# Optimization experiments

Hardware: AMD Instinct MI355X
Metric: run time of the kernel (lower is better)

## Reference

```python
import jax, jax.numpy as jnp
import numpy as np

B, T, D, H, O = 64, 4096, 256, 256, 256

def setup_inputs() -> dict:
    key = jax.random.key(0)
    kx, k1, k2, k3 = jax.random.split(key, 4)
    return {
        "x": jax.random.normal(kx, (B, T, D), dtype=jnp.float32),
        "h0": jnp.zeros((B, H), dtype=jnp.float32),
        "W_xh": jax.random.normal(k1, (D, H), dtype=jnp.float32) * 0.1,
        "W_hh": jax.random.normal(k2, (H, H), dtype=jnp.float32) * 0.1,
        "b_h": jnp.zeros((H,), dtype=jnp.float32),
        "W_hy": jax.random.normal(k3, (H, O), dtype=jnp.float32) * 0.1,
        "b_y": jnp.zeros((O,), dtype=jnp.float32),
    }

def reference(x, h0, W_xh, W_hh, b_h, W_hy, b_y):
    # Precompute input projection for all timesteps: (T, B, H)
    xp = jnp.einsum("btd,dh->tbh", x, W_xh) + b_h

    def step(h, xp_t):
        h_t = jnp.tanh(xp_t + h @ W_hh)  # (B, H)
        return h_t, h_t

    h_final, hs = jax.lax.scan(step, h0, xp)  # hs: (T, B, H)
    outputs = jnp.einsum("tbh,ho->bto", hs, W_hy) + b_y  # (B, T, O)
    return outputs, h_final
```

## Files before the change

### kernel.cpp

```cpp
#include <hip/hip_runtime.h>
#include <hip/hip_bf16.h>
#include <stdint.h>

#define TT 4096
#define BBATCH 64
#define DD 256
#define HH 256
#define OO 256

typedef float  f32x4  __attribute__((ext_vector_type(4)));
typedef short  bf16x8 __attribute__((ext_vector_type(8)));

__device__ __forceinline__ unsigned short f2bf(float f) {
  unsigned u = __float_as_uint(f);
  u += 0x7FFFu + ((u >> 16) & 1u);
  return (unsigned short)(u >> 16);
}
__device__ __forceinline__ float bf2f(unsigned short h) {
  return __uint_as_float(((unsigned)h) << 16);
}

__global__ void k0_transpose(const float* __restrict__ Wxh, const float* __restrict__ Why,
                             unsigned short* __restrict__ Wt1, unsigned short* __restrict__ Wt2) {
  const int n = blockIdx.x & 255;
  const int k = threadIdx.x;
  if (blockIdx.x < 256) Wt1[n * 256 + k] = f2bf(Wxh[k * 256 + n]);
  else                  Wt2[n * 256 + k] = f2bf(Why[k * 256 + n]);
}

__global__ __launch_bounds__(256) void k1_gemm_xp(
    const float* __restrict__ x, const unsigned short* __restrict__ Wt,
    const float* __restrict__ bh, unsigned short* __restrict__ xp) {
  __shared__ __align__(16) unsigned short As[64 * 264];
  const int tid = threadIdx.x;
  const int m0 = blockIdx.x * 64;

  #pragma unroll
  for (int rr = 0; rr < 16; ++rr) {
    int idx = tid + rr * 256;
    int row = idx >> 6;
    int c4  = (idx & 63) << 2;
    f32x4 v = *(const f32x4*)(x + (size_t)(m0 + row) * 256 + c4);
    unsigned w0 = (unsigned)f2bf(v[0]) | ((unsigned)f2bf(v[1]) << 16);
    unsigned w1 = (unsigned)f2bf(v[2]) | ((unsigned)f2bf(v[3]) << 16);
    *(uint2*)(As + row * 264 + c4) = make_uint2(w0, w1);
  }

  const int wv = tid >> 6, ln = tid & 63, l15 = ln & 15, q = ln >> 4;

  bf16x8 bfr[4][8];
  #pragma unroll
  for (int ntl = 0; ntl < 4; ++ntl) {
    #pragma unroll
    for (int kt = 0; kt < 8; ++kt) {
      int n = (wv * 4 + ntl) * 16 + l15;
      int k = kt * 32 + q * 8;
      bfr[ntl][kt] = *(const bf16x8*)(Wt + n * 256 + k);
    }
  }
  float biasv[4];
  #pragma unroll
  for (int ntl = 0; ntl < 4; ++ntl) biasv[ntl] = bh[(wv * 4 + ntl) * 16 + l15];

  __syncthreads();

  #pragma unroll 1
  for (int ms = 0; ms < 4; ++ms) {
    bf16x8 afr[8];
    #pragma unroll
    for (int kt = 0; kt < 8; ++kt)
      afr[kt] = *(const bf16x8*)(As + (ms * 16 + l15) * 264 + kt * 32 + q * 8);
    f32x4 acc[4];
    #pragma unroll
    for (int ntl = 0; ntl < 4; ++ntl) acc[ntl] = (f32x4){0.f, 0.f, 0.f, 0.f};
    #pragma unroll
    for (int ntl = 0; ntl < 4; ++ntl) {
      #pragma unroll
      for (int kt = 0; kt < 8; ++kt)
        acc[ntl] = __builtin_amdgcn_mfma_f32_16x16x32_bf16(afr[kt], bfr[ntl][kt], acc[ntl], 0, 0, 0);
    }
    #pragma unroll
    for (int ntl = 0; ntl < 4; ++ntl) {
      int c = (wv * 4 + ntl) * 16 + l15;
      #pragma unroll
      for (int r = 0; r < 4; ++r) {
        int m = m0 + ms * 16 + q * 4 + r;
        int t = m & 4095, b = m >> 12;
        xp[(size_t)(t * 64 + b) * 256 + c] = f2bf(acc[ntl][r] + biasv[ntl]);
      }
    }
  }
}

__global__ __launch_bounds__(512) void k2_rnn(
    unsigned short* xp_hs,
    const float* __restrict__ h0, const float* __restrict__ Whh,
    float* __restrict__ hfin) {
  __shared__ float hbuf[256];
  __shared__ float part[8][256];
  const int tid = threadIdx.x;
  const int b   = blockIdx.x;
  const int ig  = tid >> 6;
  const int jg  = tid & 63;

  float w[32][4];
  #pragma unroll
  for (int i = 0; i < 32; ++i)
    *(f32x4*)w[i] = *(const f32x4*)(Whh + (size_t)(32 * ig + i) * 256 + 4 * jg);

  float xpv = 0.f;
  if (tid < 256) {
    hbuf[tid] = h0[b * 256 + tid];
    xpv = bf2f(xp_hs[(size_t)b * 256 + tid]);
  }
  __syncthreads();

  #pragma unroll 1
  for (int t = 0; t < 4096; ++t) {
    float hv = hbuf[32 * ig + (tid & 31)];
    float a0 = 0.f, a1 = 0.f, a2 = 0.f, a3 = 0.f;
    #pragma unroll
    for (int i = 0; i < 32; ++i) {
      float s = __uint_as_float((unsigned)__builtin_amdgcn_readlane(__float_as_uint(hv), i));
      a0 = fmaf(s, w[i][0], a0);
      a1 = fmaf(s, w[i][1], a1);
      a2 = fmaf(s, w[i][2], a2);
      a3 = fmaf(s, w[i][3], a3);
    }
    *(f32x4*)&part[ig][4 * jg] = (f32x4){a0, a1, a2, a3};
    __syncthreads();
    if (tid < 256) {
      float s = part[0][tid] + part[1][tid] + part[2][tid] + part[3][tid]
              + part[4][tid] + part[5][tid] + part[6][tid] + part[7][tid] + xpv;
      float e  = __expf(2.f * s);
      float hn = 1.f - 2.f / (e + 1.f);
      hbuf[tid] = hn;
      xp_hs[(size_t)(t * 64 + b) * 256 + tid] = f2bf(hn);
      if (t < 4095)
        xpv = bf2f(xp_hs[(size_t)((t + 1) * 64 + b) * 256 + tid]);
    }
    __syncthreads();
  }
  if (tid < 256) hfin[b * 256 + tid] = hbuf[tid];
}

__global__ __launch_bounds__(256) void k3_gemm_out(
    const unsigned short* __restrict__ hs, const unsigned short* __restrict__ Wt,
    const float* __restrict__ by, float* __restrict__ out) {
  __shared__ __align__(16) unsigned short As[64 * 264];
  const int tid = threadIdx.x;
  const int m0 = blockIdx.x * 64;

  #pragma unroll
  for (int rr = 0; rr < 8; ++rr) {
    int idx = tid + rr * 256;
    int row = idx >> 5;
    int c8  = (idx & 31) << 3;
    *(uint4*)(As + row * 264 + c8) = *(const uint4*)(hs + (size_t)(m0 + row) * 256 + c8);
  }

  const int wv = tid >> 6, ln = tid & 63, l15 = ln & 15, q = ln >> 4;

  bf16x8 bfr[4][8];
  #pragma unroll
  for (int ntl = 0; ntl < 4; ++ntl) {
    #pragma unroll
    for (int kt = 0; kt < 8; ++kt) {
      int n = (wv * 4 + ntl) * 16 + l15;
      int k = kt * 32 + q * 8;
      bfr[ntl][kt] = *(const bf16x8*)(Wt + n * 256 + k);
    }
  }
  float biasv[4];
  #pragma unroll
  for (int ntl = 0; ntl < 4; ++ntl) biasv[ntl] = by[(wv * 4 + ntl) * 16 + l15];

  __syncthreads();

  #pragma unroll 1
  for (int ms = 0; ms < 4; ++ms) {
    bf16x8 afr[8];
    #pragma unroll
    for (int kt = 0; kt < 8; ++kt)
      afr[kt] = *(const bf16x8*)(As + (ms * 16 + l15) * 264 + kt * 32 + q * 8);
    f32x4 acc[4];
    #pragma unroll
    for (int ntl = 0; ntl < 4; ++ntl) acc[ntl] = (f32x4){0.f, 0.f, 0.f, 0.f};
    #pragma unroll
    for (int ntl = 0; ntl < 4; ++ntl) {
      #pragma unroll
      for (int kt = 0; kt < 8; ++kt)
        acc[ntl] = __builtin_amdgcn_mfma_f32_16x16x32_bf16(afr[kt], bfr[ntl][kt], acc[ntl], 0, 0, 0);
    }
    #pragma unroll
    for (int ntl = 0; ntl < 4; ++ntl) {
      int c = (wv * 4 + ntl) * 16 + l15;
      #pragma unroll
      for (int r = 0; r < 4; ++r) {
        int m  = m0 + ms * 16 + q * 4 + r;
        int bb = m & 63, t = m >> 6;
        out[(size_t)(bb * 4096 + t) * 256 + c] = acc[ntl][r] + biasv[ntl];
      }
    }
  }
}

extern "C" void kernel_launch(void* const* d_in, const int* in_sizes, int n_in,
                              void* d_out, int out_size, void* d_ws, size_t ws_size,
                              hipStream_t stream) {
  const float* x   = (const float*)d_in[0];
  const float* h0  = (const float*)d_in[1];
  const float* Wxh = (const float*)d_in[2];
  const float* Whh = (const float*)d_in[3];
  const float* bh  = (const float*)d_in[4];
  const float* Why = (const float*)d_in[5];
  const float* by  = (const float*)d_in[6];
  float* out = (float*)d_out;

  unsigned short* xp  = (unsigned short*)d_ws;
  unsigned short* Wt1 = xp + (size_t)TT * BBATCH * HH;
  unsigned short* Wt2 = Wt1 + 256 * 256;
  float* hfin = out + (size_t)BBATCH * TT * OO;

  hipLaunchKernelGGL(k0_transpose, dim3(512), dim3(256), 0, stream, Wxh, Why, Wt1, Wt2);
  hipLaunchKernelGGL(k1_gemm_xp,  dim3(4096), dim3(256), 0, stream, x, Wt1, bh, xp);
  hipLaunchKernelGGL(k2_rnn,      dim3(64),   dim3(512), 0, stream, xp, h0, Whh, hfin);
  hipLaunchKernelGGL(k3_gemm_out, dim3(4096), dim3(256), 0, stream, xp, Wt2, by, out);
}
```

Before: 4.793 ms.

## Run RNN recurrence on MFMA with 16 batches per block

Replaces the per-batch scalar-FMA recurrence kernel (64 blocks of 512 threads, one batch each, two barriers per step) with an MFMA-based kernel. Each of 4 blocks handles 16 batch rows, keeps the transposed bf16 W_hh in registers, and double-buffers the hidden state in LDS so each step needs only one barrier. The kernel also prefetches the next step's input projection and uses a reciprocal-based tanh. The trade is far fewer CUs in use and bf16 hidden-state precision in the recurrence, in exchange for much less per-step instruction and synchronisation cost.

After: 4.864 ms. Within noise of the previous version (+1.5%).

```diff
diff --git a/kernel.cpp b/kernel.cpp
--- a/kernel.cpp
+++ b/kernel.cpp
@@ -10,6 +10,7 @@
 
 typedef float  f32x4  __attribute__((ext_vector_type(4)));
 typedef short  bf16x8 __attribute__((ext_vector_type(8)));
+typedef unsigned short u16x4 __attribute__((ext_vector_type(4)));
 
 __device__ __forceinline__ unsigned short f2bf(float f) {
   unsigned u = __float_as_uint(f);
@@ -19,13 +20,25 @@
 __device__ __forceinline__ float bf2f(unsigned short h) {
   return __uint_as_float(((unsigned)h) << 16);
 }
+__device__ __forceinline__ float tanh_fast(float s) {
+  float e = __expf(2.f * s);
+  return fmaf(-2.f, __builtin_amdgcn_rcpf(e + 1.f), 1.f);
+}
+union BU { __hip_bfloat162 h2; unsigned u; };
+__device__ __forceinline__ unsigned pack_bf2(float a, float b) {
+  BU x; x.h2 = __float22bfloat162_rn(make_float2(a, b));
+  return x.u;
+}
 
 __global__ void k0_transpose(const float* __restrict__ Wxh, const float* __restrict__ Why,
-                             unsigned short* __restrict__ Wt1, unsigned short* __restrict__ Wt2) {
+                             const float* __restrict__ Whh,
+                             unsigned short* __restrict__ Wt1, unsigned short* __restrict__ Wt2,
+                             unsigned short* __restrict__ Wt3) {
   const int n = blockIdx.x & 255;
   const int k = threadIdx.x;
-  if (blockIdx.x < 256) Wt1[n * 256 + k] = f2bf(Wxh[k * 256 + n]);
-  else                  Wt2[n * 256 + k] = f2bf(Why[k * 256 + n]);
+  const float* src = (blockIdx.x < 256) ? Wxh : (blockIdx.x < 512 ? Why : Whh);
+  unsigned short* dst = (blockIdx.x < 256) ? Wt1 : (blockIdx.x < 512 ? Wt2 : Wt3);
+  dst[n * 256 + k] = f2bf(src[k * 256 + n]);
 }
 
 __global__ __launch_bounds__(256) void k1_gemm_xp(
@@ -92,56 +105,97 @@
   }
 }
 
-__global__ __launch_bounds__(512) void k2_rnn(
+#define LROW 264
+__global__ __launch_bounds__(256, 1) void k2_rnn_mfma(
     unsigned short* xp_hs,
-    const float* __restrict__ h0, const float* __restrict__ Whh,
+    const float* __restrict__ h0,
+    const unsigned short* __restrict__ Whh_t,
     float* __restrict__ hfin) {
-  __shared__ float hbuf[256];
-  __shared__ float part[8][256];
+  __shared__ __align__(16) unsigned short hbuf[2][16 * LROW];
   const int tid = threadIdx.x;
-  const int b   = blockIdx.x;
-  const int ig  = tid >> 6;
-  const int jg  = tid & 63;
-
-  float w[32][4];
-  #pragma unroll
-  for (int i = 0; i < 32; ++i)
-    *(f32x4*)w[i] = *(const f32x4*)(Whh + (size_t)(32 * ig + i) * 256 + 4 * jg);
-
-  float xpv = 0.f;
-  if (tid < 256) {
-    hbuf[tid] = h0[b * 256 + tid];
-    xpv = bf2f(xp_hs[(size_t)b * 256 + tid]);
-  }
+  const int wv  = tid >> 6;
+  const int ln  = tid & 63, l15 = ln & 15, q = ln >> 4;
+  const int bb  = blockIdx.x * 16;
+  const int b   = bb + l15;
+
+  bf16x8 wf[4][8];
+  #pragma unroll
+  for (int i = 0; i < 4; ++i)
+    #pragma unroll
+    for (int kt = 0; kt < 8; ++kt)
+      wf[i][kt] = *(const bf16x8*)(Whh_t + (size_t)((wv * 4 + i) * 16 + l15) * 256 + kt * 32 + q * 8);
+
+  {
+    int r = tid >> 4, c0i = (tid & 15) * 16;
+    const float* src = h0 + (size_t)(bb + r) * 256 + c0i;
+    #pragma unroll
+    for (int j = 0; j < 4; ++j) {
+      f32x4 v = *(const f32x4*)(src + 4 * j);
+      unsigned lo = (unsigned)f2bf(v[0]) | ((unsigned)f2bf(v[1]) << 16);
+      unsigned hi = (unsigned)f2bf(v[2]) | ((unsigned)f2bf(v[3]) << 16);
+      *(uint2*)(&hbuf[0][r * LROW + c0i + 4 * j]) = make_uint2(lo, hi);
+    }
+  }
+
+  u16x4 xpn[4];
+  #pragma unroll
+  for (int i = 0; i < 4; ++i)
+    xpn[i] = *(const u16x4*)(xp_hs + (size_t)b * 256 + (wv * 4 + i) * 16 + 4 * q);
+
   __syncthreads();
 
+  int cur = 0;
   #pragma unroll 1
-  for (int t = 0; t < 4096; ++t) {
-    float hv = hbuf[32 * ig + (tid & 31)];
-    float a0 = 0.f, a1 = 0.f, a2 = 0.f, a3 = 0.f;
-    #pragma unroll
-    for (int i = 0; i < 32; ++i) {
-      float s = __uint_as_float((unsigned)__builtin_amdgcn_readlane(__float_as_uint(hv), i));
-      a0 = fmaf(s, w[i][0], a0);
-      a1 = fmaf(s, w[i][1], a1);
-      a2 = fmaf(s, w[i][2], a2);
-      a3 = fmaf(s, w[i][3], a3);
-    }
-    *(f32x4*)&part[ig][4 * jg] = (f32x4){a0, a1, a2, a3};
-    __syncthreads();
-    if (tid < 256) {
-      float s = part[0][tid] + part[1][tid] + part[2][tid] + part[3][tid]
-              + part[4][tid] + part[5][tid] + part[6][tid] + part[7][tid] + xpv;
-      float e  = __expf(2.f * s);
-      float hn = 1.f - 2.f / (e + 1.f);
-      hbuf[tid] = hn;
-      xp_hs[(size_t)(t * 64 + b) * 256 + tid] = f2bf(hn);
-      if (t < 4095)
-        xpv = bf2f(xp_hs[(size_t)((t + 1) * 64 + b) * 256 + tid]);
-    }
-    __syncthreads();
-  }
-  if (tid < 256) hfin[b * 256 + tid] = hbuf[tid];
+  for (int t = 0; t < TT; ++t) {
+    bf16x8 hb[8];
+    #pragma unroll
+    for (int kt = 0; kt < 8; ++kt)
+      hb[kt] = *(const bf16x8*)(&hbuf[cur][l15 * LROW + kt * 32 + q * 8]);
+
+    f32x4 acc[4];
+    #pragma unroll
+    for (int i = 0; i < 4; ++i) acc[i] = (f32x4){0.f, 0.f, 0.f, 0.f};
+    #pragma unroll
+    for (int kt = 0; kt < 8; ++kt) {
+      #pragma unroll
+      for (int i = 0; i < 4; ++i)
+        acc[i] = __builtin_amdgcn_mfma_f32_16x16x32_bf16(wf[i][kt], hb[kt], acc[i], 0, 0, 0);
+    }
+
+    u16x4 xpc[4];
+    #pragma unroll
+    for (int i = 0; i < 4; ++i) xpc[i] = xpn[i];
+    if (t + 1 < TT) {
+      const unsigned short* p = xp_hs + ((size_t)(t + 1) * 64 + b) * 256;
+      #pragma unroll
+      for (int i = 0; i < 4; ++i)
+        xpn[i] = *(const u16x4*)(p + (wv * 4 + i) * 16 + 4 * q);
+    }
+
+    unsigned short* wrow  = &hbuf[cur ^ 1][l15 * LROW];
+    unsigned short* hsrow = xp_hs + ((size_t)t * 64 + b) * 256;
+    #pragma unroll
+    for (int i = 0; i < 4; ++i) {
+      const int c0 = (wv * 4 + i) * 16 + 4 * q;
+      float v0 = tanh_fast(acc[i][0] + bf2f(xpc[i][0]));
+      float v1 = tanh_fast(acc[i][1] + bf2f(xpc[i][1]));
+      float v2 = tanh_fast(acc[i][2] + bf2f(xpc[i][2]));
+      float v3 = tanh_fast(acc[i][3] + bf2f(xpc[i][3]));
+      uint2 pk = make_uint2(pack_bf2(v0, v1), pack_bf2(v2, v3));
+      *(uint2*)(wrow + c0)  = pk;
+      *(uint2*)(hsrow + c0) = pk;
+      if (t == TT - 1) {
+        hfin[(size_t)b * 256 + c0 + 0] = v0;
+        hfin[(size_t)b * 256 + c0 + 1] = v1;
+        hfin[(size_t)b * 256 + c0 + 2] = v2;
+        hfin[(size_t)b * 256 + c0 + 3] = v3;
+      }
+    }
+    asm volatile("s_waitcnt lgkmcnt(0)" ::: "memory");
+    __builtin_amdgcn_s_barrier();
+    __builtin_amdgcn_sched_barrier(0);
+    cur ^= 1;
+  }
 }
 
 __global__ __launch_bounds__(256) void k3_gemm_out(
@@ -220,10 +274,11 @@
   unsigned short* xp  = (unsigned short*)d_ws;
   unsigned short* Wt1 = xp + (size_t)TT * BBATCH * HH;
   unsigned short* Wt2 = Wt1 + 256 * 256;
+  unsigned short* Wt3 = Wt2 + 256 * 256;
   float* hfin = out + (size_t)BBATCH * TT * OO;
 
-  hipLaunchKernelGGL(k0_transpose, dim3(512), dim3(256), 0, stream, Wxh, Why, Wt1, Wt2);
-  hipLaunchKernelGGL(k1_gemm_xp,  dim3(4096), dim3(256), 0, stream, x, Wt1, bh, xp);
-  hipLaunchKernelGGL(k2_rnn,      dim3(64),   dim3(512), 0, stream, xp, h0, Whh, hfin);
-  hipLaunchKernelGGL(k3_gemm_out, dim3(4096), dim3(256), 0, stream, xp, Wt2, by, out);
-}
+  hipLaunchKernelGGL(k0_transpose, dim3(768), dim3(256), 0, stream, Wxh, Why, Whh, Wt1, Wt2, Wt3);
+  hipLaunchKernelGGL(k1_gemm_xp,   dim3(4096), dim3(256), 0, stream, x, Wt1, bh, xp);
+  hipLaunchKernelGGL(k2_rnn_mfma,  dim3(4),    dim3(256), 0, stream, xp, h0, Wt3, hfin);
+  hipLaunchKernelGGL(k3_gemm_out,  dim3(4096), dim3(256), 0, stream, xp, Wt2, by, out);
+}
```
